# Optimization experiments

Hardware: AMD Instinct MI355X
Metric: run time of the kernel (lower is better)

Reference implementation:

```python
import jax, jax.numpy as jnp
import numpy as np

H = 70  # hidden size == input size


def _renorm_rows(w, max_norm=1.0, eps=1e-7):
    # emulate nn.Embedding(max_norm=1.0): clip row L2 norm to <= 1
    n = jnp.linalg.norm(w, axis=-1, keepdims=True)
    return jnp.where(n > max_norm, w * (max_norm / (n + eps)), w)


def _lstm(x, w_ih, w_hh, b_ih, b_hh):
    # x: (B, T, H). PyTorch gate order: i, f, g, o.
    B = x.shape[0]
    xg = jnp.einsum('bth,gh->btg', x, w_ih) + (b_ih + b_hh)  # (B, T, 4H)
    def step(carry, xt):
        h, c = carry
        gates = xt + h @ w_hh.T  # (B, 4H)
        i, f, g, o = jnp.split(gates, 4, axis=-1)
        i = jax.nn.sigmoid(i); f = jax.nn.sigmoid(f)
        g = jnp.tanh(g); o = jax.nn.sigmoid(o)
        c = f * c + i * g
        h = o * jnp.tanh(c)
        return (h, c), h
    h0 = jnp.zeros((B, H), x.dtype)
    (_, _), hs = jax.lax.scan(step, (h0, h0), jnp.swapaxes(xg, 0, 1))
    return jnp.swapaxes(hs, 0, 1)  # (B, T, H)


def setup_inputs() -> dict:
    key = jax.random.key(0)
    ks = jax.random.split(key, 12)
    B, S, C = 128, 512, 1104
    s = 0.1
    return {
        'x': jax.random.uniform(ks[0], (B, S, C), jnp.float32),
        'embed_w': jax.random.normal(ks[1], (C, H), jnp.float32),
        'w_ih': jax.random.normal(ks[2], (4 * H, H), jnp.float32) * s,
        'w_hh': jax.random.normal(ks[3], (4 * H, H), jnp.float32) * s,
        'b_ih': jax.random.normal(ks[4], (4 * H,), jnp.float32) * s,
        'b_hh': jax.random.normal(ks[5], (4 * H,), jnp.float32) * s,
        'attn_w1': jax.random.normal(ks[6], (64, H), jnp.float32) * s,
        'attn_b1': jax.random.normal(ks[7], (64,), jnp.float32) * s,
        'attn_w2': jax.random.normal(ks[8], (1, 64), jnp.float32) * s,
        'attn_b2': jax.random.normal(ks[9], (1,), jnp.float32) * s,
        'fc_w': jax.random.normal(ks[10], (3, H), jnp.float32) * s,
        'fc_b': jax.random.normal(ks[11], (3,), jnp.float32) * s,
    }


def reference(x, embed_w, w_ih, w_hh, b_ih, b_hh, attn_w1, attn_b1, attn_w2, attn_b2, fc_w, fc_b):
    w = _renorm_rows(embed_w)                      # (C, H)
    # fused form of (x[...,None] * weight).sum(dim=2): plain GEMM
    e = jnp.einsum('bsc,ch->bsh', x, w)            # (B, S, H)
    out = _lstm(e, w_ih, w_hh, b_ih, b_hh)         # (B, S, H)
    # self-attention pooling
    energy = jax.nn.relu(out @ attn_w1.T + attn_b1) @ attn_w2.T + attn_b2  # (B,S,1)
    weights = jax.nn.softmax(energy[..., 0], axis=1)                        # (B,S)
    pooled = jnp.einsum('bsh,bs->bh', out, weights)                         # (B,H)
    # dropout is identity at eval
    logits = pooled @ fc_w.T + fc_b
    return jax.nn.softmax(logits, axis=1)
```

## Files before the change

### kernel.cpp

```cpp
#include <hip/hip_runtime.h>
#include <math.h>

#define HDIM 70
#define HPAD 72
#define GATES 280
#define NG 288
#define TLEN 512
#define BATCH 128
#define CDIM 1104
#define KW 1152
#define ROWS 65536

#define OFF_WRN   0
#define OFF_BIAS  77312
#define OFF_WCT   77632
#define OFF_XG    243520
#define OFF_HOUT  9418560
#define OFF_EN    14137152

typedef short short8 __attribute__((ext_vector_type(8)));
typedef float f32x4 __attribute__((ext_vector_type(4)));

__device__ __forceinline__ unsigned short f2bf(float f) {
    unsigned int u = __float_as_uint(f);
    u = (u + 0x7fffu + ((u >> 16) & 1u)) >> 16;
    return (unsigned short)u;
}
__device__ __forceinline__ float bf2f(unsigned short s) {
    return __uint_as_float(((unsigned int)s) << 16);
}

__global__ __launch_bounds__(64) void k_renorm(const float* __restrict__ w,
                                               float* __restrict__ wrn) {
    const int row = blockIdx.x;
    const int lane = threadIdx.x;
    const float* wr = w + row * HDIM;
    float v0 = wr[lane];
    float v1 = (lane < 6) ? wr[64 + lane] : 0.0f;
    float ss = v0 * v0 + v1 * v1;
    #pragma unroll
    for (int off = 32; off > 0; off >>= 1) ss += __shfl_down(ss, off);
    float tot = __shfl(ss, 0);
    float n = sqrtf(tot);
    float scale = (n > 1.0f) ? 1.0f / (n + 1e-7f) : 1.0f;
    wrn[row * HDIM + lane] = v0 * scale;
    if (lane < 6) wrn[row * HDIM + 64 + lane] = v1 * scale;
}

__global__ __launch_bounds__(256) void k_prep(const float* __restrict__ wrn,
                                              const float* __restrict__ w_ih,
                                              const float* __restrict__ b_ih,
                                              const float* __restrict__ b_hh,
                                              unsigned short* __restrict__ wcT,
                                              float* __restrict__ bias) {
    const int n = blockIdx.x;
    const int tid = threadIdx.x;
    float wr[HDIM];
    if (n < GATES) {
        #pragma unroll
        for (int h = 0; h < HDIM; ++h) wr[h] = w_ih[n * HDIM + h];
        if (tid == 0) bias[n] = b_ih[n] + b_hh[n];
    } else {
        #pragma unroll
        for (int h = 0; h < HDIM; ++h) wr[h] = 0.0f;
    }
    for (int c = tid; c < KW; c += 256) {
        float a = 0.0f;
        if (n < GATES && c < CDIM) {
            const float* wc = wrn + c * HDIM;
            #pragma unroll
            for (int h = 0; h < HDIM; ++h) a += wr[h] * wc[h];
        }
        wcT[(size_t)n * KW + c] = f2bf(a);
    }
}

__global__ __launch_bounds__(256, 2) void k_xg_gemm(const float* __restrict__ x,
                                                    const unsigned short* __restrict__ wcT,
                                                    const float* __restrict__ bias,
                                                    unsigned short* __restrict__ xg) {
    __shared__ __align__(16) unsigned short A_lds[128 * 72];
    __shared__ __align__(16) unsigned short B_lds[NG * 72];
    const int tid = threadIdx.x;
    const int lane = tid & 63;
    const int w = tid >> 6;
    const int mh = (w >> 1) * 64;
    const int nh = (w & 1) * 144;
    const int l15 = lane & 15;
    const int q = lane >> 4;
    const size_t rbase = (size_t)blockIdx.x * 128;

    f32x4 acc[4][9];
    #pragma unroll
    for (int mt = 0; mt < 4; ++mt)
        #pragma unroll
        for (int nt = 0; nt < 9; ++nt) acc[mt][nt] = (f32x4){0.f, 0.f, 0.f, 0.f};

    const int r_st = tid >> 1;
    const int kh_st = (tid & 1) * 32;

    for (int kc = 0; kc < 18; ++kc) {
        const int k0 = kc * 64;
        {
            const float* xr = x + (rbase + r_st) * (size_t)CDIM + k0 + kh_st;
            unsigned short* dst = &A_lds[r_st * 72 + kh_st];
            #pragma unroll
            for (int qq = 0; qq < 8; ++qq) {
                const int kk = k0 + kh_st + qq * 4;
                float4 v = make_float4(0.f, 0.f, 0.f, 0.f);
                if (kk < CDIM) v = *(const float4*)(xr + qq * 4);
                unsigned int lo = (unsigned int)f2bf(v.x) | ((unsigned int)f2bf(v.y) << 16);
                unsigned int hi = (unsigned int)f2bf(v.z) | ((unsigned int)f2bf(v.w) << 16);
                uint2 pv; pv.x = lo; pv.y = hi;
                *(uint2*)&dst[qq * 4] = pv;
            }
        }
        {
            #pragma unroll
            for (int p = 0; p < 9; ++p) {
                const int cid = tid + p * 256;
                const int n = cid >> 3;
                const int ko = (cid & 7) * 8;
                uint4 v = *(const uint4*)(wcT + (size_t)n * KW + k0 + ko);
                *(uint4*)&B_lds[n * 72 + ko] = v;
            }
        }
        __syncthreads();
        #pragma unroll
        for (int ks = 0; ks < 2; ++ks) {
            short8 a[4];
            short8 bfr[9];
            #pragma unroll
            for (int mt = 0; mt < 4; ++mt)
                a[mt] = *(const short8*)&A_lds[(mh + mt * 16 + l15) * 72 + ks * 32 + q * 8];
            #pragma unroll
            for (int nt = 0; nt < 9; ++nt)
                bfr[nt] = *(const short8*)&B_lds[(nh + nt * 16 + l15) * 72 + ks * 32 + q * 8];
            #pragma unroll
            for (int mt = 0; mt < 4; ++mt)
                #pragma unroll
                for (int nt = 0; nt < 9; ++nt)
                    acc[mt][nt] = __builtin_amdgcn_mfma_f32_16x16x32_bf16(a[mt], bfr[nt], acc[mt][nt], 0, 0, 0);
        }
        __syncthreads();
    }
    #pragma unroll
    for (int nt = 0; nt < 9; ++nt) {
        const int n_g = nh + nt * 16 + l15;
        if (n_g >= GATES) continue;
        const float bv = bias[n_g];
        #pragma unroll
        for (int mt = 0; mt < 4; ++mt) {
            #pragma unroll
            for (int r = 0; r < 4; ++r) {
                const size_t row = rbase + mh + mt * 16 + q * 4 + r;
                xg[row * GATES + n_g] = f2bf(acc[mt][nt][r] + bv);
            }
        }
    }
}

__device__ __forceinline__ float tanh_fast(float v) {
    v = fminf(fmaxf(v, -20.0f), 20.0f);
    float E = __expf(2.0f * v);
    return (E - 1.0f) / (E + 1.0f);
}
__device__ __forceinline__ float sigmoid_fast(float v) {
    return 1.0f / (1.0f + __expf(-v));
}

#define PF 8
__global__ __launch_bounds__(320) void k_lstm(const unsigned short* __restrict__ xg,
                                              const float* __restrict__ w_hh,
                                              float* __restrict__ hout) {
    __shared__ __align__(16) float h_lds[HPAD];
    __shared__ float gates_lds[GATES];
    const int tid = threadIdx.x;
    const int b = blockIdx.x;
    float whh[HPAD];
    if (tid < GATES) {
        #pragma unroll
        for (int j = 0; j < HDIM; ++j) whh[j] = w_hh[tid * HDIM + j];
        whh[70] = whh[71] = 0.0f;
    } else {
        #pragma unroll
        for (int j = 0; j < HPAD; ++j) whh[j] = 0.0f;
    }
    if (tid < HPAD) h_lds[tid] = 0.0f;
    float c_reg = 0.0f;

    const unsigned short* xp = xg + (size_t)b * TLEN * GATES + (tid < GATES ? tid : 0);
    float xbuf[PF];
    #pragma unroll
    for (int i = 0; i < PF; ++i) xbuf[i] = bf2f(xp[i * GATES]);
    __syncthreads();

    #pragma unroll 8
    for (int t = 0; t < TLEN; ++t) {
        const int slot = t & (PF - 1);
        const float xcur = xbuf[slot];
        xbuf[slot] = bf2f(xp[((t + PF) & (TLEN - 1)) * GATES]);
        float a0 = 0.f, a1 = 0.f, a2 = 0.f, a3 = 0.f;
        #pragma unroll
        for (int jj = 0; jj < 18; ++jj) {
            float4 hv = ((const float4*)h_lds)[jj];
            a0 += hv.x * whh[4 * jj];
            a1 += hv.y * whh[4 * jj + 1];
            a2 += hv.z * whh[4 * jj + 2];
            a3 += hv.w * whh[4 * jj + 3];
        }
        const float acc = xcur + ((a0 + a1) + (a2 + a3));
        if (tid < GATES) {
            float a;
            if (tid < 140)      a = sigmoid_fast(acc);
            else if (tid < 210) a = tanh_fast(acc);
            else                a = sigmoid_fast(acc);
            gates_lds[tid] = a;
        }
        __syncthreads();
        if (tid < HDIM) {
            const float iv = gates_lds[tid];
            const float fv = gates_lds[tid + 70];
            const float gv = gates_lds[tid + 140];
            const float ov = gates_lds[tid + 210];
            c_reg = fv * c_reg + iv * gv;
            const float hn = ov * tanh_fast(c_reg);
            h_lds[tid] = hn;
            hout[((size_t)b * TLEN + t) * HPAD + tid] = hn;
        }
        __syncthreads();
    }
}

__global__ __launch_bounds__(256) void k_energy(const float* __restrict__ hout,
                                                const float* __restrict__ w1,
                                                const float* __restrict__ b1,
                                                const float* __restrict__ w2,
                                                const float* __restrict__ b2,
                                                float* __restrict__ energy) {
    const int lane = threadIdx.x & 63;
    const int wid = blockIdx.x * 4 + (threadIdx.x >> 6);
    float w1r[HPAD];
    #pragma unroll
    for (int c = 0; c < HDIM; ++c) w1r[c] = w1[lane * HDIM + c];
    w1r[70] = w1r[71] = 0.0f;
    const float b1v = b1[lane];
    const float w2v = w2[lane];
    const float b2v = b2[0];
    for (int row = wid; row < ROWS; row += 4096) {
        const float4* rp = (const float4*)(hout + (size_t)row * HPAD);
        float a0 = 0.f, a1 = 0.f, a2 = 0.f, a3 = 0.f;
        #pragma unroll
        for (int jj = 0; jj < 18; ++jj) {
            float4 v = rp[jj];
            a0 += v.x * w1r[4 * jj];
            a1 += v.y * w1r[4 * jj + 1];
            a2 += v.z * w1r[4 * jj + 2];
            a3 += v.w * w1r[4 * jj + 3];
        }
        float hid = fmaxf((a0 + a1) + (a2 + a3) + b1v, 0.0f) * w2v;
        #pragma unroll
        for (int off = 32; off > 0; off >>= 1) hid += __shfl_down(hid, off);
        if (lane == 0) energy[row] = hid + b2v;
    }
}

__global__ __launch_bounds__(128) void k_pool(const float* __restrict__ hout,
                                              const float* __restrict__ energy,
                                              const float* __restrict__ fc_w,
                                              const float* __restrict__ fc_b,
                                              float* __restrict__ outp) {
    __shared__ float red[128];
    __shared__ float wexp[TLEN];
    __shared__ float pooledL[HDIM];
    const int tid = threadIdx.x;
    const int b = blockIdx.x;
    float v[4];
    #pragma unroll
    for (int k = 0; k < 4; ++k) v[k] = energy[b * TLEN + tid + 128 * k];
    float m = fmaxf(fmaxf(v[0], v[1]), fmaxf(v[2], v[3]));
    red[tid] = m; __syncthreads();
    for (int s = 64; s > 0; s >>= 1) {
        if (tid < s) red[tid] = fmaxf(red[tid], red[tid + s]);
        __syncthreads();
    }
    const float M = red[0]; __syncthreads();
    float s4 = 0.f;
    #pragma unroll
    for (int k = 0; k < 4; ++k) {
        float ex = __expf(v[k] - M);
        wexp[tid + 128 * k] = ex;
        s4 += ex;
    }
    red[tid] = s4; __syncthreads();
    for (int s = 64; s > 0; s >>= 1) {
        if (tid < s) red[tid] += red[tid + s];
        __syncthreads();
    }
    const float rinv = 1.0f / red[0];
    if (tid < HDIM) {
        float a0 = 0.f, a1 = 0.f, a2 = 0.f, a3 = 0.f;
        const float* hp = hout + (size_t)b * TLEN * HPAD + tid;
        for (int s = 0; s < TLEN; s += 4) {
            a0 += wexp[s]     * hp[(size_t)(s)     * HPAD];
            a1 += wexp[s + 1] * hp[(size_t)(s + 1) * HPAD];
            a2 += wexp[s + 2] * hp[(size_t)(s + 2) * HPAD];
            a3 += wexp[s + 3] * hp[(size_t)(s + 3) * HPAD];
        }
        pooledL[tid] = ((a0 + a1) + (a2 + a3)) * rinv;
    }
    __syncthreads();
    if (tid == 0) {
        float l[3];
        #pragma unroll
        for (int i = 0; i < 3; ++i) {
            float a = fc_b[i];
            for (int h = 0; h < HDIM; ++h) a += fc_w[i * HDIM + h] * pooledL[h];
            l[i] = a;
        }
        float m3 = fmaxf(l[0], fmaxf(l[1], l[2]));
        float e0 = __expf(l[0] - m3), e1 = __expf(l[1] - m3), e2 = __expf(l[2] - m3);
        float rs = 1.0f / (e0 + e1 + e2);
        outp[b * 3 + 0] = e0 * rs;
        outp[b * 3 + 1] = e1 * rs;
        outp[b * 3 + 2] = e2 * rs;
    }
}

extern "C" void kernel_launch(void* const* d_in, const int* in_sizes, int n_in,
                              void* d_out, int out_size, void* d_ws, size_t ws_size,
                              hipStream_t stream) {
    const float* x       = (const float*)d_in[0];
    const float* embed_w = (const float*)d_in[1];
    const float* w_ih    = (const float*)d_in[2];
    const float* w_hh    = (const float*)d_in[3];
    const float* b_ih    = (const float*)d_in[4];
    const float* b_hh    = (const float*)d_in[5];
    const float* aw1     = (const float*)d_in[6];
    const float* ab1     = (const float*)d_in[7];
    const float* aw2     = (const float*)d_in[8];
    const float* ab2     = (const float*)d_in[9];
    const float* fc_w    = (const float*)d_in[10];
    const float* fc_b    = (const float*)d_in[11];
    float* outp = (float*)d_out;
    float* ws = (float*)d_ws;

    float* wrn  = ws + OFF_WRN;
    float* bias = ws + OFF_BIAS;
    unsigned short* wcT = (unsigned short*)(ws + OFF_WCT);
    unsigned short* xgp = (unsigned short*)(ws + OFF_XG);
    float* ho = ws + OFF_HOUT;
    float* en = ws + OFF_EN;

    k_renorm<<<CDIM, 64, 0, stream>>>(embed_w, wrn);
    k_prep<<<NG, 256, 0, stream>>>(wrn, w_ih, b_ih, b_hh, wcT, bias);
    k_xg_gemm<<<512, 256, 0, stream>>>(x, wcT, bias, xgp);
    k_lstm<<<BATCH, 320, 0, stream>>>(xgp, w_hh, ho);
    k_energy<<<1024, 256, 0, stream>>>(ho, aw1, ab1, aw2, ab2, en);
    k_pool<<<BATCH, 128, 0, stream>>>(ho, en, fc_w, fc_b, outp);
}
```

Baseline: 861.9 us.

## Restructure LSTM step to one barrier using quad-split hidden dot and shuffles

The LSTM recurrence is reorganized so each group of four threads owns one hidden unit. Each thread computes a 20-wide slice of the dot product for all four gates, the slices are combined with xor shuffles, and the cell update runs in-register. This removes the gates LDS round trip and one of the two barriers per timestep, and double-buffers h. To support this, the input projection now writes gates interleaved per unit. The renorm output is also transposed so k_prep reads are coalesced.

```diff
diff --git a/kernel.cpp b/kernel.cpp
--- a/kernel.cpp
+++ b/kernel.cpp
@@ -3,6 +3,7 @@
 
 #define HDIM 70
 #define HPAD 72
+#define HP2 80
 #define GATES 280
 #define NG 288
 #define TLEN 512
@@ -11,7 +12,7 @@
 #define KW 1152
 #define ROWS 65536
 
-#define OFF_WRN   0
+#define OFF_WRNT  0
 #define OFF_BIAS  77312
 #define OFF_WCT   77632
 #define OFF_XG    243520
@@ -31,7 +32,7 @@
 }
 
 __global__ __launch_bounds__(64) void k_renorm(const float* __restrict__ w,
-                                               float* __restrict__ wrn) {
+                                               float* __restrict__ wrnT) {
     const int row = blockIdx.x;
     const int lane = threadIdx.x;
     const float* wr = w + row * HDIM;
@@ -43,11 +44,11 @@
     float tot = __shfl(ss, 0);
     float n = sqrtf(tot);
     float scale = (n > 1.0f) ? 1.0f / (n + 1e-7f) : 1.0f;
-    wrn[row * HDIM + lane] = v0 * scale;
-    if (lane < 6) wrn[row * HDIM + 64 + lane] = v1 * scale;
-}
-
-__global__ __launch_bounds__(256) void k_prep(const float* __restrict__ wrn,
+    wrnT[lane * CDIM + row] = v0 * scale;
+    if (lane < 6) wrnT[(64 + lane) * CDIM + row] = v1 * scale;
+}
+
+__global__ __launch_bounds__(256) void k_prep(const float* __restrict__ wrnT,
                                               const float* __restrict__ w_ih,
                                               const float* __restrict__ b_ih,
                                               const float* __restrict__ b_hh,
@@ -67,9 +68,8 @@
     for (int c = tid; c < KW; c += 256) {
         float a = 0.0f;
         if (n < GATES && c < CDIM) {
-            const float* wc = wrn + c * HDIM;
-            #pragma unroll
-            for (int h = 0; h < HDIM; ++h) a += wr[h] * wc[h];
+            #pragma unroll
+            for (int h = 0; h < HDIM; ++h) a += wr[h] * wrnT[h * CDIM + c];
         }
         wcT[(size_t)n * KW + c] = f2bf(a);
     }
@@ -87,7 +87,7 @@
     const int mh = (w >> 1) * 64;
     const int nh = (w & 1) * 144;
     const int l15 = lane & 15;
-    const int q = lane >> 4;
+    const int lq = lane >> 4;
     const size_t rbase = (size_t)blockIdx.x * 128;
 
     f32x4 acc[4][9];
@@ -132,10 +132,10 @@
             short8 bfr[9];
             #pragma unroll
             for (int mt = 0; mt < 4; ++mt)
-                a[mt] = *(const short8*)&A_lds[(mh + mt * 16 + l15) * 72 + ks * 32 + q * 8];
+                a[mt] = *(const short8*)&A_lds[(mh + mt * 16 + l15) * 72 + ks * 32 + lq * 8];
             #pragma unroll
             for (int nt = 0; nt < 9; ++nt)
-                bfr[nt] = *(const short8*)&B_lds[(nh + nt * 16 + l15) * 72 + ks * 32 + q * 8];
+                bfr[nt] = *(const short8*)&B_lds[(nh + nt * 16 + l15) * 72 + ks * 32 + lq * 8];
             #pragma unroll
             for (int mt = 0; mt < 4; ++mt)
                 #pragma unroll
@@ -149,12 +149,15 @@
         const int n_g = nh + nt * 16 + l15;
         if (n_g >= GATES) continue;
         const float bv = bias[n_g];
+        const int comp = n_g / 70;
+        const int unit = n_g - comp * 70;
+        const int col = unit * 4 + comp;
         #pragma unroll
         for (int mt = 0; mt < 4; ++mt) {
             #pragma unroll
             for (int r = 0; r < 4; ++r) {
-                const size_t row = rbase + mh + mt * 16 + q * 4 + r;
-                xg[row * GATES + n_g] = f2bf(acc[mt][nt][r] + bv);
+                const size_t row = rbase + mh + mt * 16 + lq * 4 + r;
+                xg[row * GATES + col] = f2bf(acc[mt][nt][r] + bv);
             }
         }
     }
@@ -173,60 +176,66 @@
 __global__ __launch_bounds__(320) void k_lstm(const unsigned short* __restrict__ xg,
                                               const float* __restrict__ w_hh,
                                               float* __restrict__ hout) {
-    __shared__ __align__(16) float h_lds[HPAD];
-    __shared__ float gates_lds[GATES];
+    __shared__ __align__(16) float h_lds[2][HP2];
     const int tid = threadIdx.x;
     const int b = blockIdx.x;
-    float whh[HPAD];
-    if (tid < GATES) {
-        #pragma unroll
-        for (int j = 0; j < HDIM; ++j) whh[j] = w_hh[tid * HDIM + j];
-        whh[70] = whh[71] = 0.0f;
-    } else {
-        #pragma unroll
-        for (int j = 0; j < HPAD; ++j) whh[j] = 0.0f;
-    }
-    if (tid < HPAD) h_lds[tid] = 0.0f;
+    const int q = tid >> 2;
+    const int c = tid & 3;
+
+    float whh[4][20];
+    #pragma unroll
+    for (int v = 0; v < 4; ++v)
+        #pragma unroll
+        for (int kk = 0; kk < 20; ++kk) {
+            const int k = 20 * c + kk;
+            whh[v][kk] = (q < HDIM && k < HDIM) ? w_hh[(70 * v + q) * HDIM + k] : 0.0f;
+        }
+
+    if (tid < HP2) { h_lds[0][tid] = 0.0f; h_lds[1][tid] = 0.0f; }
     float c_reg = 0.0f;
 
     const unsigned short* xp = xg + (size_t)b * TLEN * GATES + (tid < GATES ? tid : 0);
     float xbuf[PF];
     #pragma unroll
-    for (int i = 0; i < PF; ++i) xbuf[i] = bf2f(xp[i * GATES]);
+    for (int i = 0; i < PF; ++i) xbuf[i] = bf2f(xp[(size_t)i * GATES]);
     __syncthreads();
 
     #pragma unroll 8
     for (int t = 0; t < TLEN; ++t) {
         const int slot = t & (PF - 1);
         const float xcur = xbuf[slot];
-        xbuf[slot] = bf2f(xp[((t + PF) & (TLEN - 1)) * GATES]);
-        float a0 = 0.f, a1 = 0.f, a2 = 0.f, a3 = 0.f;
-        #pragma unroll
-        for (int jj = 0; jj < 18; ++jj) {
-            float4 hv = ((const float4*)h_lds)[jj];
-            a0 += hv.x * whh[4 * jj];
-            a1 += hv.y * whh[4 * jj + 1];
-            a2 += hv.z * whh[4 * jj + 2];
-            a3 += hv.w * whh[4 * jj + 3];
-        }
-        const float acc = xcur + ((a0 + a1) + (a2 + a3));
-        if (tid < GATES) {
-            float a;
-            if (tid < 140)      a = sigmoid_fast(acc);
-            else if (tid < 210) a = tanh_fast(acc);
-            else                a = sigmoid_fast(acc);
-            gates_lds[tid] = a;
-        }
-        __syncthreads();
-        if (tid < HDIM) {
-            const float iv = gates_lds[tid];
-            const float fv = gates_lds[tid + 70];
-            const float gv = gates_lds[tid + 140];
-            const float ov = gates_lds[tid + 210];
-            c_reg = fv * c_reg + iv * gv;
-            const float hn = ov * tanh_fast(c_reg);
-            h_lds[tid] = hn;
-            hout[((size_t)b * TLEN + t) * HPAD + tid] = hn;
+        xbuf[slot] = bf2f(xp[(size_t)((t + PF) & (TLEN - 1)) * GATES]);
+
+        float acc[4] = {0.f, 0.f, 0.f, 0.f};
+        const float4* hp = (const float4*)&h_lds[t & 1][20 * c];
+        #pragma unroll
+        for (int i5 = 0; i5 < 5; ++i5) {
+            const float4 hv = hp[i5];
+            #pragma unroll
+            for (int v = 0; v < 4; ++v) {
+                acc[v] += hv.x * whh[v][4 * i5];
+                acc[v] += hv.y * whh[v][4 * i5 + 1];
+                acc[v] += hv.z * whh[v][4 * i5 + 2];
+                acc[v] += hv.w * whh[v][4 * i5 + 3];
+            }
+        }
+        acc[c] += xcur;
+
+        #pragma unroll
+        for (int v = 0; v < 4; ++v) {
+            acc[v] += __shfl_xor(acc[v], 1);
+            acc[v] += __shfl_xor(acc[v], 2);
+        }
+
+        const float iv = sigmoid_fast(acc[0]);
+        const float fv = sigmoid_fast(acc[1]);
+        const float gv = tanh_fast(acc[2]);
+        const float ov = sigmoid_fast(acc[3]);
+        c_reg = fv * c_reg + iv * gv;
+        const float hn = ov * tanh_fast(c_reg);
+        if (c == 0) {
+            h_lds[(t & 1) ^ 1][q] = hn;
+            if (q < HDIM) hout[((size_t)b * TLEN + t) * HPAD + q] = hn;
         }
         __syncthreads();
     }
@@ -242,7 +251,7 @@
     const int wid = blockIdx.x * 4 + (threadIdx.x >> 6);
     float w1r[HPAD];
     #pragma unroll
-    for (int c = 0; c < HDIM; ++c) w1r[c] = w1[lane * HDIM + c];
+    for (int cc = 0; cc < HDIM; ++cc) w1r[cc] = w1[lane * HDIM + cc];
     w1r[70] = w1r[71] = 0.0f;
     const float b1v = b1[lane];
     const float w2v = w2[lane];
@@ -345,15 +354,15 @@
     float* outp = (float*)d_out;
     float* ws = (float*)d_ws;
 
-    float* wrn  = ws + OFF_WRN;
+    float* wrnT = ws + OFF_WRNT;
     float* bias = ws + OFF_BIAS;
     unsigned short* wcT = (unsigned short*)(ws + OFF_WCT);
     unsigned short* xgp = (unsigned short*)(ws + OFF_XG);
     float* ho = ws + OFF_HOUT;
     float* en = ws + OFF_EN;
 
-    k_renorm<<<CDIM, 64, 0, stream>>>(embed_w, wrn);
-    k_prep<<<NG, 256, 0, stream>>>(wrn, w_ih, b_ih, b_hh, wcT, bias);
+    k_renorm<<<CDIM, 64, 0, stream>>>(embed_w, wrnT);
+    k_prep<<<NG, 256, 0, stream>>>(wrnT, w_ih, b_ih, b_hh, wcT, bias);
     k_xg_gemm<<<512, 256, 0, stream>>>(x, wcT, bias, xgp);
     k_lstm<<<BATCH, 320, 0, stream>>>(xgp, w_hh, ho);
     k_energy<<<1024, 256, 0, stream>>>(ho, aw1, ab1, aw2, ab2, en);
```

New measurement: 890.0 us. 1.03x slower.
